# Kernel optimization log

Hardware: AMD Instinct MI355X
Metric: run time of the kernel (lower is better)

Reference implementation:

```python
import jax, jax.numpy as jnp
import numpy as np

N, F, E, A, H = 50000, 64, 1600000, 8, 16
RECEPTIVE_FIELD = 7


def setup_inputs() -> dict:
    key = jax.random.key(0)
    ks = jax.random.split(key, 12)
    inp = {
        "x": jax.random.normal(ks[0], (N, F), dtype=jnp.float32),
        "edge_index": jax.random.randint(ks[1], (2, E), 0, N, dtype=jnp.int64),
        "w1": jax.random.normal(ks[2], (F, H), dtype=jnp.float32) * 0.1,
        "b1": jax.random.normal(ks[3], (H,), dtype=jnp.float32) * 0.1,
        "w2": jax.random.normal(ks[4], (H, H), dtype=jnp.float32) * 0.1,
        "b2": jax.random.normal(ks[5], (H,), dtype=jnp.float32) * 0.1,
        "w3": jax.random.normal(ks[6], (H, F), dtype=jnp.float32) * 0.1,
        "b3": jax.random.normal(ks[7], (F,), dtype=jnp.float32) * 0.1,
        "fc1_w": jax.random.normal(ks[8], ((1 + RECEPTIVE_FIELD) * F, F), dtype=jnp.float32) * 0.05,
        "fc1_b": jax.random.normal(ks[9], (F,), dtype=jnp.float32) * 0.05,
        "fc2_w": jax.random.normal(ks[10], (F, A), dtype=jnp.float32) * 0.1,
        "fc2_b": jax.random.normal(ks[11], (A,), dtype=jnp.float32) * 0.1,
    }
    return inp


def _mlp(x, w1, b1, w2, b2, w3, b3):
    h = jax.nn.relu(x @ w1 + b1)
    h = jax.nn.relu(h @ w2 + b2)
    return h @ w3 + b3


def _agg_mean(x, src, dst):
    # scatter-mean: mean of source-node features over incoming edges per target
    s = jax.ops.segment_sum(x[src], dst, num_segments=N)          # [N, F]
    cnt = jax.ops.segment_sum(jnp.ones((src.shape[0], 1), x.dtype), dst, num_segments=N)
    return s / jnp.maximum(cnt, 1.0)  # nodes with no in-edges -> 0 (torch mean aggr)


def reference(x, edge_index, w1, b1, w2, b2, w3, b3, fc1_w, fc1_b, fc2_w, fc2_b):
    src, dst = edge_index[0], edge_index[1]
    mlp = lambda t: _mlp(t, w1, b1, w2, b2, w3, b3)
    fields = [mlp(mlp(x))]
    for i in range(RECEPTIVE_FIELD):
        x_ = mlp(x)
        for _ in range(i + 1):
            x_ = _agg_mean(x_, src, dst)
        fields.append(mlp(x_))
    f = jnp.concatenate(fields, axis=1)          # [N, 8*F]
    h = f @ fc1_w + fc1_b                        # [N, F]
    logits = h @ fc2_w + fc2_b                   # [N, A]
    return jax.nn.softmax(logits, axis=-1)       # Categorical probs
```

## Files before the change

kernel.cpp:

```cpp
#include <hip/hip_runtime.h>
#include <hip/hip_fp16.h>


#define NB2MAX 400
#define NBLK   256
#define CAP2   32
#define CAPC   48
#define CAPB   6144
#define OVCAP  1024
#define LCAP   6144
#define CAPN   64

__global__ __launch_bounds__(1024) void binfill_k(
    const int* __restrict__ src, const int* __restrict__ dst, int E, int n,
    int* __restrict__ gcur, int* __restrict__ ovbuf,
    int* __restrict__ bins, int* __restrict__ cnts,
    const float* __restrict__ w1, const float* __restrict__ w3,
    const float* __restrict__ b3, const float* __restrict__ fc1w,
    const float* __restrict__ fc1b, const float* __restrict__ fc2w,
    const float* __restrict__ fc2b,
    float* __restrict__ M, float* __restrict__ cvec,
    float* __restrict__ W31, float* __restrict__ c31) {
    __shared__ int lbuf[NB2MAX * CAP2];
    __shared__ int lcnt[NB2MAX];
    __shared__ int lflush[NB2MAX];
    int tid = threadIdx.x;
    int NB = (n + 127) >> 7;

    if ((int)blockIdx.x >= NBLK) {
        float* fl = (float*)lbuf;
        int s = (int)blockIdx.x - NBLK;
        if (s == 0) {
            if (tid < 256) {
                int i = tid >> 4, j = tid & 15;
                float a = 0.f;
                for (int g = 0; g < 64; g++) a += w3[i * 64 + g] * w1[g * 16 + j];
                W31[tid] = a;
            } else if (tid < 272) {
                int j = tid - 256;
                float a = 0.f;
                for (int g = 0; g < 64; g++) a += b3[g] * w1[g * 16 + j];
                c31[j] = a;
            } else if (tid >= 320 && tid < 384) {
                int h = tid - 320;
                float a = 0.f;
                for (int r = 0; r < 512; r++) a += b3[r & 63] * fc1w[r * 64 + h];
                fl[h] = a;
            }
            __syncthreads();
            if (tid < 8) {
                float a = fc2b[tid];
                for (int h = 0; h < 64; h++) a += (fc1b[h] + fl[h]) * fc2w[h * 8 + tid];
                cvec[tid] = a;
            }
        } else {
            int k = s - 1;
            {
                int i = tid >> 6, h = tid & 63;
                float a = 0.f;
                const float* f1 = fc1w + (size_t)(k * 64) * 64 + h;
                for (int g = 0; g < 64; g++) a += w3[i * 64 + g] * f1[g * 64];
                fl[i * 64 + h] = a;
            }
            __syncthreads();
            if (tid < 128) {
                int i = tid >> 3, j = tid & 7;
                float a = 0.f;
                for (int h = 0; h < 64; h++) a += fl[i * 64 + h] * fc2w[h * 8 + j];
                M[k * 128 + i * 8 + j] = a;
            }
        }
        return;
    }

    for (int b = tid; b < NB; b += 1024) { lcnt[b] = 0; lflush[b] = 0; }
    __syncthreads();
    int blk = blockIdx.x;
    int chunk = (E + NBLK - 1) / NBLK;
    int beg = blk * chunk;
    int end = beg + chunk; if (end > E) end = E;
    for (int t0 = beg; t0 < end; t0 += 1024) {
        int e = t0 + tid;
        if (e < end) {
            int d = dst[e], s = src[e];
            if ((unsigned)d < (unsigned)n && (unsigned)s < (unsigned)n) {
                int b = d >> 7;
                int pk = ((d & 127) << 16) | s;
                int pos = atomicAdd(&lcnt[b], 1);
                if (pos < CAP2) lbuf[b * CAP2 + pos] = pk;
                else {
                    int p = atomicAdd(&gcur[b], 1);
                    if (p < OVCAP) ovbuf[b * OVCAP + p] = pk;
                }
            }
        }
        __syncthreads();
        for (int b = tid; b < NB; b += 1024) {
            int cnt = lcnt[b]; if (cnt > CAP2) cnt = CAP2;
            int fl2 = lflush[b];
            size_t cell = ((size_t)b * NBLK + blk) * CAPC;
            int base = 0;
            while (cnt - base >= 16) {
                if (fl2 + 16 <= CAPC) {
                    int* dp = bins + cell + fl2;
                    #pragma unroll
                    for (int q = 0; q < 16; q++) dp[q] = lbuf[b * CAP2 + base + q];
                    fl2 += 16;
                } else {
                    int p = atomicAdd(&gcur[b], 16);
                    for (int q = 0; q < 16; q++)
                        if (p + q < OVCAP) ovbuf[b * OVCAP + p + q] = lbuf[b * CAP2 + base + q];
                }
                base += 16;
            }
            int rem = cnt - base;
            if (base > 0)
                for (int q = 0; q < rem; q++) lbuf[b * CAP2 + q] = lbuf[b * CAP2 + base + q];
            lcnt[b] = rem; lflush[b] = fl2;
        }
        __syncthreads();
    }
    for (int b = tid; b < NB; b += 1024) {
        int cnt = lcnt[b]; if (cnt > CAP2) cnt = CAP2;
        int fl2 = lflush[b];
        size_t cell = ((size_t)b * NBLK + blk) * CAPC;
        if (fl2 + cnt <= CAPC) {
            for (int q = 0; q < cnt; q++) bins[cell + fl2 + q] = lbuf[b * CAP2 + q];
            fl2 += cnt;
        } else {
            int p = atomicAdd(&gcur[b], cnt);
            for (int q = 0; q < cnt; q++)
                if (p + q < OVCAP) ovbuf[b * OVCAP + p + q] = lbuf[b * CAP2 + q];
        }
        cnts[(size_t)blk * NB + b] = fl2;
    }
}

__global__ __launch_bounds__(256) void csr2_k(
    const int* __restrict__ bins, const int* __restrict__ cnts,
    const int* __restrict__ gcur, const int* __restrict__ ovbuf,
    unsigned short* __restrict__ csrp_s, int2* __restrict__ nd_s,
    int* __restrict__ csr, int2* __restrict__ be, int* __restrict__ lcnt3,
    int n) {
    __shared__ int hist[128], pref[128], cur[128], slot[128];
    __shared__ int scnt[NBLK];
    __shared__ int lbuf[LCAP];
    __shared__ int sov;
    __shared__ int ccnt[3], cbase[3];
    int tid = threadIdx.x;
    int NB = (n + 127) >> 7;
    int b = blockIdx.x;
    if (tid < 128) { hist[tid] = 0; cur[tid] = 0; }
    if (tid < 3) ccnt[tid] = 0;
    scnt[tid] = cnts[(size_t)tid * NB + b];
    if (tid == 0) {
        int g = gcur[b];
        sov = g < 0 ? 0 : (g > OVCAP ? OVCAP : g);
    }
    __syncthreads();
    {
        int c = scnt[tid];
        size_t cell = ((size_t)b * NBLK + tid) * CAPC;
        for (int i = 0; i < c; i++) atomicAdd(&hist[bins[cell + i] >> 16], 1);
    }
    if (tid == 0)
        for (int i = 0; i < sov; i++) atomicAdd(&hist[ovbuf[b * OVCAP + i] >> 16], 1);
    __syncthreads();
    if (tid == 0) {
        int r = 0;
        for (int i = 0; i < 128; i++) { pref[i] = r; r += hist[i]; }
    }
    __syncthreads();
    {
        int c = scnt[tid];
        size_t cell = ((size_t)b * NBLK + tid) * CAPC;
        for (int i = 0; i < c; i++) {
            int pk = bins[cell + i];
            int dl = pk >> 16;
            int pos = pref[dl] + atomicAdd(&cur[dl], 1);
            if (pos < LCAP) lbuf[pos] = pk & 0xffff;
        }
    }
    if (tid == 0) {
        for (int i = 0; i < sov; i++) {
            int pk = ovbuf[b * OVCAP + i];
            int dl = pk >> 16;
            int pos = pref[dl] + atomicAdd(&cur[dl], 1);
            if (pos < LCAP) lbuf[pos] = pk & 0xffff;
        }
    }
    __syncthreads();
    int myc = -1, lpos = 0;
    if (tid < 128) {
        int d = (b << 7) + tid;
        if (d < n) {
            int cnt = hist[tid];
            myc = cnt <= 32 ? 0 : (cnt <= 48 ? 1 : 2);
            lpos = atomicAdd(&ccnt[myc], 1);
        }
    }
    __syncthreads();
    if (tid < 3) cbase[tid] = atomicAdd(&lcnt3[tid], ccnt[tid]);
    __syncthreads();
    if (myc >= 0) {
        int d = (b << 7) + tid;
        int cnt = hist[tid];
        int s = myc * n + cbase[myc] + lpos;
        slot[tid] = s;
        nd_s[s] = make_int2(d, cnt);
        if (cnt > CAPN) {
            int s0 = b * CAPB + pref[tid];
            be[d] = make_int2(s0 + CAPN, s0 + cnt);
            for (int j = CAPN; j < cnt; j++)
                csr[s0 + j] = lbuf[pref[tid] + j] << 2;
        }
    }
    __syncthreads();
    for (int q = tid; q < 128 * CAPN; q += 256) {
        int dl = q >> 6, j = q & 63;
        int d = (b << 7) + dl;
        if (d >= n) break;
        int cnt = hist[dl];
        int v = (j < cnt) ? lbuf[pref[dl] + j] : n;
        int pos = ((j & 3) << 4) | (j >> 2);
        csrp_s[(size_t)slot[dl] * CAPN + pos] = (unsigned short)v;
    }
}

__device__ __forceinline__ void acc_row(uint2 u, float& ax, float& ay,
                                        float& az, float& aw) {
    __half2 p = *reinterpret_cast<const __half2*>(&u.x);
    __half2 q = *reinterpret_cast<const __half2*>(&u.y);
    float2 f = __half22float2(p), g = __half22float2(q);
    ax += f.x; ay += f.y; az += g.x; aw += g.y;
}

__global__ __launch_bounds__(256) void proj_k(
    const float* __restrict__ x, __half* __restrict__ z0, __half* __restrict__ z1,
    float* __restrict__ logits,
    const float* __restrict__ w1, const float* __restrict__ b1,
    const float* __restrict__ w2, const float* __restrict__ b2,
    const float* __restrict__ W31, const float* __restrict__ c31,
    const float* __restrict__ M0, const float* __restrict__ cvec, int n) {
    __shared__ float sw1[1024], sw2[256], sW[256], sM[128];
    __shared__ float sb1[16], sb2[16], sc[16], scv[8];
    int tid = threadIdx.x;
    for (int i = tid; i < 1024; i += 256) sw1[i] = w1[i];
    sw2[tid] = w2[tid & 255];
    sW[tid & 255] = W31[tid & 255];
    if (tid < 128) sM[tid] = M0[tid];
    if (tid < 16) { sb1[tid] = b1[tid]; sb2[tid] = b2[tid]; sc[tid] = c31[tid]; }
    if (tid < 8) scv[tid] = cvec[tid];
    __syncthreads();
    if (blockIdx.x == 0 && tid < 16) {
        ((unsigned short*)z0)[(size_t)n * 16 + tid] = 0;
        ((unsigned short*)z1)[(size_t)n * 16 + tid] = 0;
    }
    int nid = blockIdx.x * 256 + tid;
    if (nid >= n) return;
    float t1[16];
    #pragma unroll
    for (int j = 0; j < 16; j++) t1[j] = sb1[j];
    const float4* xp = (const float4*)(x + (size_t)nid * 64);
    #pragma unroll
    for (int q = 0; q < 16; q++) {
        float4 v = xp[q];
        #pragma unroll
        for (int j = 0; j < 16; j++)
            t1[j] += v.x * sw1[(4 * q) * 16 + j] + v.y * sw1[(4 * q + 1) * 16 + j]
                   + v.z * sw1[(4 * q + 2) * 16 + j] + v.w * sw1[(4 * q + 3) * 16 + j];
    }
    #pragma unroll
    for (int j = 0; j < 16; j++) t1[j] = fmaxf(t1[j], 0.f);
    float t2[16];
    #pragma unroll
    for (int j = 0; j < 16; j++) {
        float a = sb2[j];
        #pragma unroll
        for (int i = 0; i < 16; i++) a += t1[i] * sw2[i * 16 + j];
        t2[j] = fmaxf(a, 0.f);
    }
    float z[16];
    #pragma unroll
    for (int j = 0; j < 16; j++) {
        float a = sc[j];
        #pragma unroll
        for (int i = 0; i < 16; i++) a += t2[i] * sW[i * 16 + j];
        z[j] = a;
    }
    __half2* zo = (__half2*)(z0 + (size_t)nid * 16);
    #pragma unroll
    for (int q = 0; q < 8; q++)
        zo[q] = __floats2half2_rn(z[2 * q], z[2 * q + 1]);
    float h[16], f2[16];
    #pragma unroll
    for (int i = 0; i < 16; i++) h[i] = fmaxf(z[i] + sb1[i], 0.f);
    #pragma unroll
    for (int j = 0; j < 16; j++) {
        float a = sb2[j];
        #pragma unroll
        for (int i = 0; i < 16; i++) a += h[i] * sw2[i * 16 + j];
        f2[j] = fmaxf(a, 0.f);
    }
    float* lp = logits + (size_t)nid * 8;
    #pragma unroll
    for (int j = 0; j < 8; j++) {
        float l = scv[j];
        #pragma unroll
        for (int i = 0; i < 16; i++) l += f2[i] * sM[i * 8 + j];
        lp[j] = l;
    }
}

__global__ __launch_bounds__(256, 4) void hop_k(
    const __half* __restrict__ zin, __half* __restrict__ zout,
    float* __restrict__ logits,
    const unsigned short* __restrict__ csrp_s, const int2* __restrict__ nd_s,
    const int2* __restrict__ be, const int* __restrict__ csr,
    const int* __restrict__ lcnt3,
    const float* __restrict__ w2, const float* __restrict__ b1,
    const float* __restrict__ b2, const float* __restrict__ M, int n, int FB) {
    __shared__ float sw2[256], sM[128], sb1[16], sb2[16];
    int tid = threadIdx.x;
    if ((int)blockIdx.x < FB) {
        sw2[tid] = w2[tid];
        if (tid < 128) sM[tid] = M[tid];
        if (tid < 16) { sb1[tid] = b1[tid]; sb2[tid] = b2[tid]; }
        __syncthreads();
        int nid = blockIdx.x * 256 + tid;
        if (nid >= n) return;
        float h[16];
        const __half2* zp = (const __half2*)(zin + (size_t)nid * 16);
        #pragma unroll
        for (int q = 0; q < 8; q++) {
            float2 f = __half22float2(zp[q]);
            h[2 * q] = f.x; h[2 * q + 1] = f.y;
        }
        #pragma unroll
        for (int i = 0; i < 16; i++) h[i] = fmaxf(h[i] + sb1[i], 0.f);
        float t2[16];
        #pragma unroll
        for (int j = 0; j < 16; j++) {
            float a = sb2[j];
            #pragma unroll
            for (int i = 0; i < 16; i++) a += h[i] * sw2[i * 16 + j];
            t2[j] = fmaxf(a, 0.f);
        }
        float* lp = logits + (size_t)nid * 8;
        #pragma unroll
        for (int j = 0; j < 8; j++) {
            float l = 0.f;
            #pragma unroll
            for (int i = 0; i < 16; i++) l += t2[i] * sM[i * 8 + j];
            lp[j] += l;
        }
        return;
    }
    int wave = tid >> 6;
    int lane = tid & 63;
    int quarter = lane >> 4;
    int l16 = lane & 15;
    int t4 = l16 >> 2, ch = l16 & 3;
    int idx = (((int)blockIdx.x - FB) * 4 + wave) * 4 + quarter;
    if (idx >= n) return;
    int ns = lcnt3[0], nm = lcnt3[1];
    int tier; size_t row;
    if (idx < ns)           { tier = 0; row = (size_t)idx; }
    else if (idx < ns + nm) { tier = 1; row = (size_t)n + (idx - ns); }
    else                    { tier = 2; row = 2 * (size_t)n + (idx - ns - nm); }
    int2 nd = nd_s[row];
    int node = nd.x, degi = nd.y;
    const uint4* ip = (const uint4*)(csrp_s + (row << 6));
    uint4 pa = ip[t4 * 2];
    int r0 = pa.x & 0xffff, r1 = pa.x >> 16;
    int r2 = pa.y & 0xffff, r3 = pa.y >> 16;
    int r4 = pa.z & 0xffff, r5 = pa.z >> 16;
    int r6 = pa.w & 0xffff, r7 = pa.w >> 16;
    const uint2* z2 = (const uint2*)zin;
    uint2 u0 = z2[((size_t)r0 << 2) + ch];
    uint2 u1 = z2[((size_t)r1 << 2) + ch];
    uint2 u2 = z2[((size_t)r2 << 2) + ch];
    uint2 u3 = z2[((size_t)r3 << 2) + ch];
    uint2 u4 = z2[((size_t)r4 << 2) + ch];
    uint2 u5 = z2[((size_t)r5 << 2) + ch];
    uint2 u6 = z2[((size_t)r6 << 2) + ch];
    uint2 u7 = z2[((size_t)r7 << 2) + ch];
    float ax = 0.f, ay = 0.f, az = 0.f, aw = 0.f;
    acc_row(u0, ax, ay, az, aw); acc_row(u1, ax, ay, az, aw);
    acc_row(u2, ax, ay, az, aw); acc_row(u3, ax, ay, az, aw);
    acc_row(u4, ax, ay, az, aw); acc_row(u5, ax, ay, az, aw);
    acc_row(u6, ax, ay, az, aw); acc_row(u7, ax, ay, az, aw);
    if (tier >= 1) {
        uint4 pb = ip[t4 * 2 + 1];
        int r8 = pb.x & 0xffff, r9 = pb.x >> 16;
        int rA = pb.y & 0xffff, rB = pb.y >> 16;
        uint2 u8 = z2[((size_t)r8 << 2) + ch];
        uint2 u9 = z2[((size_t)r9 << 2) + ch];
        uint2 uA = z2[((size_t)rA << 2) + ch];
        uint2 uB = z2[((size_t)rB << 2) + ch];
        acc_row(u8, ax, ay, az, aw); acc_row(u9, ax, ay, az, aw);
        acc_row(uA, ax, ay, az, aw); acc_row(uB, ax, ay, az, aw);
        if (tier == 2) {
            int rC = pb.z & 0xffff, rD = pb.z >> 16;
            int rE = pb.w & 0xffff, rF = pb.w >> 16;
            uint2 uC = z2[((size_t)rC << 2) + ch];
            uint2 uD = z2[((size_t)rD << 2) + ch];
            uint2 uE = z2[((size_t)rE << 2) + ch];
            uint2 uF = z2[((size_t)rF << 2) + ch];
            acc_row(uC, ax, ay, az, aw); acc_row(uD, ax, ay, az, aw);
            acc_row(uE, ax, ay, az, aw); acc_row(uF, ax, ay, az, aw);
            if (degi > CAPN) {
                int2 r = be[node];
                for (int q = r.x + t4; q < r.y; q += 4) {
                    uint2 u = z2[(size_t)csr[q] + ch];
                    acc_row(u, ax, ay, az, aw);
                }
            }
        }
    }
    #pragma unroll
    for (int off = 8; off >= 4; off >>= 1) {
        ax += __shfl_down(ax, off, 16);
        ay += __shfl_down(ay, off, 16);
        az += __shfl_down(az, off, 16);
        aw += __shfl_down(aw, off, 16);
    }
    if (l16 < 4) {
        float inv = 1.f / (float)(degi > 0 ? degi : 1);
        __half2 h01 = __floats2half2_rn(ax * inv, ay * inv);
        __half2 h23 = __floats2half2_rn(az * inv, aw * inv);
        uint2 w;
        w.x = *reinterpret_cast<unsigned int*>(&h01);
        w.y = *reinterpret_cast<unsigned int*>(&h23);
        ((uint2*)(zout + (size_t)node * 16))[l16] = w;
    }
}

__global__ __launch_bounds__(256) void fieldsoft_k(
    const __half* __restrict__ z, float* __restrict__ logits,
    const float* __restrict__ w2, const float* __restrict__ b1,
    const float* __restrict__ b2, const float* __restrict__ M, int n) {
    __shared__ float sw2[256], sM[128], sb1[16], sb2[16];
    int tid = threadIdx.x;
    sw2[tid] = w2[tid];
    if (tid < 128) sM[tid] = M[tid];
    if (tid < 16) { sb1[tid] = b1[tid]; sb2[tid] = b2[tid]; }
    __syncthreads();
    int nid = blockIdx.x * 256 + tid;
    if (nid >= n) return;
    float h[16];
    const __half2* zp = (const __half2*)(z + (size_t)nid * 16);
    #pragma unroll
    for (int q = 0; q < 8; q++) {
        float2 f = __half22float2(zp[q]);
        h[2 * q] = f.x; h[2 * q + 1] = f.y;
    }
    #pragma unroll
    for (int i = 0; i < 16; i++) h[i] = fmaxf(h[i] + sb1[i], 0.f);
    float t2[16];
    #pragma unroll
    for (int j = 0; j < 16; j++) {
        float a = sb2[j];
        #pragma unroll
        for (int i = 0; i < 16; i++) a += h[i] * sw2[i * 16 + j];
        t2[j] = fmaxf(a, 0.f);
    }
    float4* lp4 = (float4*)(logits + (size_t)nid * 8);
    float4 l0 = lp4[0], l1 = lp4[1];
    float v[8] = {l0.x, l0.y, l0.z, l0.w, l1.x, l1.y, l1.z, l1.w};
    #pragma unroll
    for (int j = 0; j < 8; j++) {
        float l = 0.f;
        #pragma unroll
        for (int i = 0; i < 16; i++) l += t2[i] * sM[i * 8 + j];
        v[j] += l;
    }
    float m = v[0];
    #pragma unroll
    for (int j = 1; j < 8; j++) m = fmaxf(m, v[j]);
    float s = 0.f;
    #pragma unroll
    for (int j = 0; j < 8; j++) { v[j] = expf(v[j] - m); s += v[j]; }
    float inv = 1.f / s;
    lp4[0] = make_float4(v[0] * inv, v[1] * inv, v[2] * inv, v[3] * inv);
    lp4[1] = make_float4(v[4] * inv, v[5] * inv, v[6] * inv, v[7] * inv);
}

extern "C" void kernel_launch(void* const* d_in, const int* in_sizes, int n_in,
                              void* d_out, int out_size, void* d_ws, size_t ws_size,
                              hipStream_t stream) {
    const float* x    = (const float*)d_in[0];
    const int*   ei   = (const int*)d_in[1];
    const float* w1   = (const float*)d_in[2];
    const float* b1   = (const float*)d_in[3];
    const float* w2   = (const float*)d_in[4];
    const float* b2   = (const float*)d_in[5];
    const float* w3   = (const float*)d_in[6];
    const float* b3   = (const float*)d_in[7];
    const float* fc1w = (const float*)d_in[8];
    const float* fc1b = (const float*)d_in[9];
    const float* fc2w = (const float*)d_in[10];
    const float* fc2b = (const float*)d_in[11];
    float* out = (float*)d_out;

    int n = in_sizes[0] / 64;
    int E = in_sizes[1] / 2;
    int NB = (n + 127) >> 7;
    const int* src = ei;
    const int* dst = ei + E;

    char* ws = (char*)d_ws;
    auto carve = [&](size_t bytes) {
        char* p = ws;
        ws += (bytes + 255) & ~((size_t)255);
        return p;
    };
    int*   gcur    = (int*)carve((size_t)NB * 4);
    int*   lcnt3   = (int*)carve(16);
    int*   ovbuf   = (int*)carve((size_t)NB * OVCAP * 4);
    int*   binsbuf = (int*)carve((size_t)NB * NBLK * CAPC * 4);
    int*   cnts    = (int*)carve((size_t)NBLK * NB * 4);
    unsigned short* csrp_s = (unsigned short*)carve((size_t)3 * n * CAPN * 2);
    int2*  nd_s    = (int2*)carve((size_t)3 * n * 8);
    int*   csr     = (int*)carve((size_t)NB * CAPB * 4);
    int2*  be      = (int2*)carve((size_t)n * 8);
    __half* buf0   = (__half*)carve((size_t)(n + 1) * 16 * 2);
    __half* buf1   = (__half*)carve((size_t)(n + 1) * 16 * 2);
    float* M       = (float*)carve(1024 * 4);
    float* cvec    = (float*)carve(8 * 4);
    float* W31     = (float*)carve(256 * 4);
    float* c31     = (float*)carve(16 * 4);

    size_t gpad = ((size_t)NB * 4 + 255) & ~((size_t)255);
    hipMemsetAsync(gcur, 0, gpad + 16, stream);
    binfill_k<<<NBLK + 9, 1024, 0, stream>>>(src, dst, E, n, gcur, ovbuf, binsbuf, cnts,
                                             w1, w3, b3, fc1w, fc1b, fc2w, fc2b,
                                             M, cvec, W31, c31);
    csr2_k<<<NB, 256, 0, stream>>>(binsbuf, cnts, gcur, ovbuf,
                                   csrp_s, nd_s, csr, be, lcnt3, n);

    int FB = (n + 255) / 256;
    int AB = (n + 15) / 16;
    proj_k<<<FB, 256, 0, stream>>>(x, buf0, buf1, out, w1, b1, w2, b2,
                                   W31, c31, M, cvec, n);

    __half* cur = buf0;
    __half* nxt = buf1;
    hop_k<<<AB, 256, 0, stream>>>(cur, nxt, out, csrp_s, nd_s, be, csr, lcnt3,
                                  w2, b1, b2, M, n, 0);
    { __half* t = cur; cur = nxt; nxt = t; }
    for (int k = 1; k <= 6; k++) {
        hop_k<<<FB + AB, 256, 0, stream>>>(cur, nxt, out, csrp_s, nd_s, be, csr,
                                           lcnt3, w2, b1, b2, M + k * 128, n, FB);
        __half* t = cur; cur = nxt; nxt = t;
    }
    fieldsoft_k<<<FB, 256, 0, stream>>>(cur, out, w2, b1, b2, M + 7 * 128, n);
}
```

Measured before the change: 240.2 us.

## Process several nodes per quarter-wave in hop kernel with prefetched CSR metadata

The aggregation part of hop_k now loops over NPW=4 nodes per 16-lane group, using a grid-stride walk, and launches a quarter as many aggregation blocks. While one node's neighbour rows are gathered, it loads the next node's degree record and packed neighbour indices. The aim is to hide the latency of those dependent metadata loads and to cut block launch and scheduling overhead. In exchange there is less parallelism, since fewer waves are in flight, and higher register pressure. The second CSR vector is now loaded even for low-degree nodes that do not need it.

```diff
diff --git a/kernel.cpp b/kernel.cpp
--- a/kernel.cpp
+++ b/kernel.cpp
@@ -10,6 +10,7 @@
 #define OVCAP  1024
 #define LCAP   6144
 #define CAPN   64
+#define NPW    4
 
 __global__ __launch_bounds__(1024) void binfill_k(
     const int* __restrict__ src, const int* __restrict__ dst, int E, int n,
@@ -361,78 +362,103 @@
     int quarter = lane >> 4;
     int l16 = lane & 15;
     int t4 = l16 >> 2, ch = l16 & 3;
-    int idx = (((int)blockIdx.x - FB) * 4 + wave) * 4 + quarter;
-    if (idx >= n) return;
+    int QTOT = (((int)gridDim.x - FB)) << 4;
+    int gq = (((int)blockIdx.x - FB) * 4 + wave) * 4 + quarter;
     int ns = lcnt3[0], nm = lcnt3[1];
-    int tier; size_t row;
-    if (idx < ns)           { tier = 0; row = (size_t)idx; }
-    else if (idx < ns + nm) { tier = 1; row = (size_t)n + (idx - ns); }
-    else                    { tier = 2; row = 2 * (size_t)n + (idx - ns - nm); }
-    int2 nd = nd_s[row];
-    int node = nd.x, degi = nd.y;
-    const uint4* ip = (const uint4*)(csrp_s + (row << 6));
-    uint4 pa = ip[t4 * 2];
-    int r0 = pa.x & 0xffff, r1 = pa.x >> 16;
-    int r2 = pa.y & 0xffff, r3 = pa.y >> 16;
-    int r4 = pa.z & 0xffff, r5 = pa.z >> 16;
-    int r6 = pa.w & 0xffff, r7 = pa.w >> 16;
     const uint2* z2 = (const uint2*)zin;
-    uint2 u0 = z2[((size_t)r0 << 2) + ch];
-    uint2 u1 = z2[((size_t)r1 << 2) + ch];
-    uint2 u2 = z2[((size_t)r2 << 2) + ch];
-    uint2 u3 = z2[((size_t)r3 << 2) + ch];
-    uint2 u4 = z2[((size_t)r4 << 2) + ch];
-    uint2 u5 = z2[((size_t)r5 << 2) + ch];
-    uint2 u6 = z2[((size_t)r6 << 2) + ch];
-    uint2 u7 = z2[((size_t)r7 << 2) + ch];
-    float ax = 0.f, ay = 0.f, az = 0.f, aw = 0.f;
-    acc_row(u0, ax, ay, az, aw); acc_row(u1, ax, ay, az, aw);
-    acc_row(u2, ax, ay, az, aw); acc_row(u3, ax, ay, az, aw);
-    acc_row(u4, ax, ay, az, aw); acc_row(u5, ax, ay, az, aw);
-    acc_row(u6, ax, ay, az, aw); acc_row(u7, ax, ay, az, aw);
-    if (tier >= 1) {
-        uint4 pb = ip[t4 * 2 + 1];
-        int r8 = pb.x & 0xffff, r9 = pb.x >> 16;
-        int rA = pb.y & 0xffff, rB = pb.y >> 16;
-        uint2 u8 = z2[((size_t)r8 << 2) + ch];
-        uint2 u9 = z2[((size_t)r9 << 2) + ch];
-        uint2 uA = z2[((size_t)rA << 2) + ch];
-        uint2 uB = z2[((size_t)rB << 2) + ch];
-        acc_row(u8, ax, ay, az, aw); acc_row(u9, ax, ay, az, aw);
-        acc_row(uA, ax, ay, az, aw); acc_row(uB, ax, ay, az, aw);
-        if (tier == 2) {
-            int rC = pb.z & 0xffff, rD = pb.z >> 16;
-            int rE = pb.w & 0xffff, rF = pb.w >> 16;
-            uint2 uC = z2[((size_t)rC << 2) + ch];
-            uint2 uD = z2[((size_t)rD << 2) + ch];
-            uint2 uE = z2[((size_t)rE << 2) + ch];
-            uint2 uF = z2[((size_t)rF << 2) + ch];
-            acc_row(uC, ax, ay, az, aw); acc_row(uD, ax, ay, az, aw);
-            acc_row(uE, ax, ay, az, aw); acc_row(uF, ax, ay, az, aw);
-            if (degi > CAPN) {
-                int2 r = be[node];
-                for (int q = r.x + t4; q < r.y; q += 4) {
-                    uint2 u = z2[(size_t)csr[q] + ch];
-                    acc_row(u, ax, ay, az, aw);
+
+    int idx = gq;
+    int tier = 0;
+    int2 nd = make_int2(0, 1);
+    uint4 pa = make_uint4(0, 0, 0, 0), pb = make_uint4(0, 0, 0, 0);
+    if (idx < n) {
+        size_t row;
+        if (idx < ns)           { tier = 0; row = (size_t)idx; }
+        else if (idx < ns + nm) { tier = 1; row = (size_t)n + (idx - ns); }
+        else                    { tier = 2; row = 2 * (size_t)n + (idx - ns - nm); }
+        nd = nd_s[row];
+        const uint4* ip = (const uint4*)(csrp_s + (row << 6));
+        pa = ip[t4 * 2];
+        pb = ip[t4 * 2 + 1];
+    }
+    #pragma unroll
+    for (int it = 0; it < NPW; ++it) {
+        int idxn = idx + QTOT;
+        int tiern = tier; int2 ndn = nd; uint4 pan = pa, pbn = pb;
+        if (it + 1 < NPW && idxn < n) {
+            size_t row;
+            if (idxn < ns)           { tiern = 0; row = (size_t)idxn; }
+            else if (idxn < ns + nm) { tiern = 1; row = (size_t)n + (idxn - ns); }
+            else                     { tiern = 2; row = 2 * (size_t)n + (idxn - ns - nm); }
+            ndn = nd_s[row];
+            const uint4* ip = (const uint4*)(csrp_s + (row << 6));
+            pan = ip[t4 * 2];
+            pbn = ip[t4 * 2 + 1];
+        }
+        if (idx < n) {
+            int node = nd.x, degi = nd.y;
+            int r0 = pa.x & 0xffff, r1 = pa.x >> 16;
+            int r2 = pa.y & 0xffff, r3 = pa.y >> 16;
+            int r4 = pa.z & 0xffff, r5 = pa.z >> 16;
+            int r6 = pa.w & 0xffff, r7 = pa.w >> 16;
+            uint2 u0 = z2[((size_t)r0 << 2) + ch];
+            uint2 u1 = z2[((size_t)r1 << 2) + ch];
+            uint2 u2 = z2[((size_t)r2 << 2) + ch];
+            uint2 u3 = z2[((size_t)r3 << 2) + ch];
+            uint2 u4 = z2[((size_t)r4 << 2) + ch];
+            uint2 u5 = z2[((size_t)r5 << 2) + ch];
+            uint2 u6 = z2[((size_t)r6 << 2) + ch];
+            uint2 u7 = z2[((size_t)r7 << 2) + ch];
+            float ax = 0.f, ay = 0.f, az = 0.f, aw = 0.f;
+            acc_row(u0, ax, ay, az, aw); acc_row(u1, ax, ay, az, aw);
+            acc_row(u2, ax, ay, az, aw); acc_row(u3, ax, ay, az, aw);
+            acc_row(u4, ax, ay, az, aw); acc_row(u5, ax, ay, az, aw);
+            acc_row(u6, ax, ay, az, aw); acc_row(u7, ax, ay, az, aw);
+            if (tier >= 1) {
+                int r8 = pb.x & 0xffff, r9 = pb.x >> 16;
+                int rA = pb.y & 0xffff, rB = pb.y >> 16;
+                uint2 u8 = z2[((size_t)r8 << 2) + ch];
+                uint2 u9 = z2[((size_t)r9 << 2) + ch];
+                uint2 uA = z2[((size_t)rA << 2) + ch];
+                uint2 uB = z2[((size_t)rB << 2) + ch];
+                acc_row(u8, ax, ay, az, aw); acc_row(u9, ax, ay, az, aw);
+                acc_row(uA, ax, ay, az, aw); acc_row(uB, ax, ay, az, aw);
+                if (tier == 2) {
+                    int rC = pb.z & 0xffff, rD = pb.z >> 16;
+                    int rE = pb.w & 0xffff, rF = pb.w >> 16;
+                    uint2 uC = z2[((size_t)rC << 2) + ch];
+                    uint2 uD = z2[((size_t)rD << 2) + ch];
+                    uint2 uE = z2[((size_t)rE << 2) + ch];
+                    uint2 uF = z2[((size_t)rF << 2) + ch];
+                    acc_row(uC, ax, ay, az, aw); acc_row(uD, ax, ay, az, aw);
+                    acc_row(uE, ax, ay, az, aw); acc_row(uF, ax, ay, az, aw);
+                    if (degi > CAPN) {
+                        int2 r = be[node];
+                        for (int q = r.x + t4; q < r.y; q += 4) {
+                            uint2 u = z2[(size_t)csr[q] + ch];
+                            acc_row(u, ax, ay, az, aw);
+                        }
+                    }
                 }
             }
-        }
-    }
-    #pragma unroll
-    for (int off = 8; off >= 4; off >>= 1) {
-        ax += __shfl_down(ax, off, 16);
-        ay += __shfl_down(ay, off, 16);
-        az += __shfl_down(az, off, 16);
-        aw += __shfl_down(aw, off, 16);
-    }
-    if (l16 < 4) {
-        float inv = 1.f / (float)(degi > 0 ? degi : 1);
-        __half2 h01 = __floats2half2_rn(ax * inv, ay * inv);
-        __half2 h23 = __floats2half2_rn(az * inv, aw * inv);
-        uint2 w;
-        w.x = *reinterpret_cast<unsigned int*>(&h01);
-        w.y = *reinterpret_cast<unsigned int*>(&h23);
-        ((uint2*)(zout + (size_t)node * 16))[l16] = w;
+            #pragma unroll
+            for (int off = 8; off >= 4; off >>= 1) {
+                ax += __shfl_down(ax, off, 16);
+                ay += __shfl_down(ay, off, 16);
+                az += __shfl_down(az, off, 16);
+                aw += __shfl_down(aw, off, 16);
+            }
+            if (l16 < 4) {
+                float inv = 1.f / (float)(degi > 0 ? degi : 1);
+                __half2 h01 = __floats2half2_rn(ax * inv, ay * inv);
+                __half2 h23 = __floats2half2_rn(az * inv, aw * inv);
+                uint2 w;
+                w.x = *reinterpret_cast<unsigned int*>(&h01);
+                w.y = *reinterpret_cast<unsigned int*>(&h23);
+                ((uint2*)(zout + (size_t)nd.x * 16))[l16] = w;
+            }
+        }
+        idx = idxn; tier = tiern; nd = ndn; pa = pan; pb = pbn;
     }
 }
 
@@ -540,7 +566,7 @@
                                    csrp_s, nd_s, csr, be, lcnt3, n);
 
     int FB = (n + 255) / 256;
-    int AB = (n + 15) / 16;
+    int AB = (n + 16 * NPW - 1) / (16 * NPW);
     proj_k<<<FB, 256, 0, stream>>>(x, buf0, buf1, out, w1, b1, w2, b2,
                                    W31, c31, M, cvec, n);
 
```

Result: slower. 251.1 us (+4.6%).

## Parallelize proj_k across 16 lanes per node with shared-memory x staging

Applied to the files above, without the earlier changes.

The projection kernel now assigns 16 threads per node, one per hidden unit, instead of one thread per node with 16-wide register arrays. Input rows are staged through padded shared memory with coalesced float4 loads, and intermediate vectors are exchanged with width-16 shuffles. The logits reduction uses xor-shuffle trees. This is meant to raise occupancy and parallelism and cut register pressure, at the cost of 16x more blocks, each reloading the weight tables into shared memory, plus extra shuffle traffic.

```diff
diff --git a/kernel.cpp b/kernel.cpp
--- a/kernel.cpp
+++ b/kernel.cpp
@@ -235,80 +235,73 @@
     ax += f.x; ay += f.y; az += g.x; aw += g.y;
 }
 
-__global__ __launch_bounds__(256) void proj_k(
+__global__ __launch_bounds__(256, 4) void proj_k(
     const float* __restrict__ x, __half* __restrict__ z0, __half* __restrict__ z1,
     float* __restrict__ logits,
     const float* __restrict__ w1, const float* __restrict__ b1,
     const float* __restrict__ w2, const float* __restrict__ b2,
     const float* __restrict__ W31, const float* __restrict__ c31,
     const float* __restrict__ M0, const float* __restrict__ cvec, int n) {
+    __shared__ float sx[16 * 68];
     __shared__ float sw1[1024], sw2[256], sW[256], sM[128];
     __shared__ float sb1[16], sb2[16], sc[16], scv[8];
     int tid = threadIdx.x;
     for (int i = tid; i < 1024; i += 256) sw1[i] = w1[i];
-    sw2[tid] = w2[tid & 255];
-    sW[tid & 255] = W31[tid & 255];
+    sw2[tid] = w2[tid];
+    sW[tid] = W31[tid];
     if (tid < 128) sM[tid] = M0[tid];
     if (tid < 16) { sb1[tid] = b1[tid]; sb2[tid] = b2[tid]; sc[tid] = c31[tid]; }
     if (tid < 8) scv[tid] = cvec[tid];
-    __syncthreads();
     if (blockIdx.x == 0 && tid < 16) {
         ((unsigned short*)z0)[(size_t)n * 16 + tid] = 0;
         ((unsigned short*)z1)[(size_t)n * 16 + tid] = 0;
     }
-    int nid = blockIdx.x * 256 + tid;
-    if (nid >= n) return;
-    float t1[16];
-    #pragma unroll
-    for (int j = 0; j < 16; j++) t1[j] = sb1[j];
-    const float4* xp = (const float4*)(x + (size_t)nid * 64);
-    #pragma unroll
-    for (int q = 0; q < 16; q++) {
-        float4 v = xp[q];
-        #pragma unroll
-        for (int j = 0; j < 16; j++)
-            t1[j] += v.x * sw1[(4 * q) * 16 + j] + v.y * sw1[(4 * q + 1) * 16 + j]
-                   + v.z * sw1[(4 * q + 2) * 16 + j] + v.w * sw1[(4 * q + 3) * 16 + j];
-    }
-    #pragma unroll
-    for (int j = 0; j < 16; j++) t1[j] = fmaxf(t1[j], 0.f);
-    float t2[16];
-    #pragma unroll
-    for (int j = 0; j < 16; j++) {
-        float a = sb2[j];
-        #pragma unroll
-        for (int i = 0; i < 16; i++) a += t1[i] * sw2[i * 16 + j];
-        t2[j] = fmaxf(a, 0.f);
-    }
-    float z[16];
-    #pragma unroll
-    for (int j = 0; j < 16; j++) {
-        float a = sc[j];
-        #pragma unroll
-        for (int i = 0; i < 16; i++) a += t2[i] * sW[i * 16 + j];
-        z[j] = a;
-    }
-    __half2* zo = (__half2*)(z0 + (size_t)nid * 16);
-    #pragma unroll
-    for (int q = 0; q < 8; q++)
-        zo[q] = __floats2half2_rn(z[2 * q], z[2 * q + 1]);
-    float h[16], f2[16];
-    #pragma unroll
-    for (int i = 0; i < 16; i++) h[i] = fmaxf(z[i] + sb1[i], 0.f);
-    #pragma unroll
-    for (int j = 0; j < 16; j++) {
-        float a = sb2[j];
-        #pragma unroll
-        for (int i = 0; i < 16; i++) a += h[i] * sw2[i * 16 + j];
-        f2[j] = fmaxf(a, 0.f);
-    }
-    float* lp = logits + (size_t)nid * 8;
-    #pragma unroll
-    for (int j = 0; j < 8; j++) {
-        float l = scv[j];
-        #pragma unroll
-        for (int i = 0; i < 16; i++) l += f2[i] * sM[i * 8 + j];
-        lp[j] = l;
+    int node0 = blockIdx.x * 16;
+    {
+        int r = tid >> 4, c4 = tid & 15;
+        if (node0 + r < n) {
+            float4 v = ((const float4*)(x + (size_t)(node0 + r) * 64))[c4];
+            float* dstp = sx + r * 68 + c4 * 4;
+            dstp[0] = v.x; dstp[1] = v.y; dstp[2] = v.z; dstp[3] = v.w;
+        }
+    }
+    __syncthreads();
+    int nl = tid >> 4, jj = tid & 15;
+    int node = node0 + nl;
+    if (node >= n) return;
+    float t1 = 0.f;
+    const float* xr = sx + nl * 68;
+    #pragma unroll
+    for (int g = 0; g < 64; g++) t1 += xr[g] * sw1[g * 16 + jj];
+    t1 = fmaxf(t1 + sb1[jj], 0.f);
+    float t2 = sb2[jj];
+    #pragma unroll
+    for (int i = 0; i < 16; i++) t2 += __shfl(t1, i, 16) * sw2[i * 16 + jj];
+    t2 = fmaxf(t2, 0.f);
+    float zv = sc[jj];
+    #pragma unroll
+    for (int i = 0; i < 16; i++) zv += __shfl(t2, i, 16) * sW[i * 16 + jj];
+    z0[(size_t)node * 16 + jj] = __float2half(zv);
+    float hv = fmaxf(zv + sb1[jj], 0.f);
+    float f2 = sb2[jj];
+    #pragma unroll
+    for (int i = 0; i < 16; i++) f2 += __shfl(hv, i, 16) * sw2[i * 16 + jj];
+    f2 = fmaxf(f2, 0.f);
+    float p0 = f2 * sM[jj * 8 + 0], p1 = f2 * sM[jj * 8 + 1];
+    float p2 = f2 * sM[jj * 8 + 2], p3 = f2 * sM[jj * 8 + 3];
+    float p4 = f2 * sM[jj * 8 + 4], p5 = f2 * sM[jj * 8 + 5];
+    float p6 = f2 * sM[jj * 8 + 6], p7 = f2 * sM[jj * 8 + 7];
+    #pragma unroll
+    for (int off = 1; off < 16; off <<= 1) {
+        p0 += __shfl_xor(p0, off, 16); p1 += __shfl_xor(p1, off, 16);
+        p2 += __shfl_xor(p2, off, 16); p3 += __shfl_xor(p3, off, 16);
+        p4 += __shfl_xor(p4, off, 16); p5 += __shfl_xor(p5, off, 16);
+        p6 += __shfl_xor(p6, off, 16); p7 += __shfl_xor(p7, off, 16);
+    }
+    if (jj < 8) {
+        float myp = jj == 0 ? p0 : jj == 1 ? p1 : jj == 2 ? p2 : jj == 3 ? p3
+                  : jj == 4 ? p4 : jj == 5 ? p5 : jj == 6 ? p6 : p7;
+        logits[(size_t)node * 8 + jj] = scv[jj] + myp;
     }
 }
 
@@ -539,10 +532,11 @@
     csr2_k<<<NB, 256, 0, stream>>>(binsbuf, cnts, gcur, ovbuf,
                                    csrp_s, nd_s, csr, be, lcnt3, n);
 
-    int FB = (n + 255) / 256;
-    int AB = (n + 15) / 16;
-    proj_k<<<FB, 256, 0, stream>>>(x, buf0, buf1, out, w1, b1, w2, b2,
-                                   W31, c31, M, cvec, n);
+    int FB  = (n + 255) / 256;
+    int FBJ = (n + 15) / 16;
+    int AB  = (n + 15) / 16;
+    proj_k<<<FBJ, 256, 0, stream>>>(x, buf0, buf1, out, w1, b1, w2, b2,
+                                    W31, c31, M, cvec, n);
 
     __half* cur = buf0;
     __half* nxt = buf1;
```

After: 243.2 us. No clear change (+1.3%).
